# Performance work log

Measured on AMD Instinct MI355X. Metric: run time of the kernel, lower is better.

Reference implementation:

```python
import jax, jax.numpy as jnp
import numpy as np

N_NODES, N_EDGES = 50000, 800000
IN_DIM, OUT_DIM, EDGE_DIM = 128, 128, 32
NUM_HEADS = 8
HEAD_DIM = OUT_DIM // NUM_HEADS
SCALE = HEAD_DIM ** -0.5


def setup_inputs() -> dict:
    key = jax.random.key(0)
    ks = jax.random.split(key, 8)
    def lin_w(k, fan_in, fan_out):
        # kaiming-uniform-ish init like nn.Linear
        bound = 1.0 / np.sqrt(fan_in)
        return jax.random.uniform(k, (fan_in, fan_out), jnp.float32, -bound, bound)
    return {
        "node_features": jax.random.normal(ks[0], (N_NODES, IN_DIM), jnp.float32),
        "edge_features": jax.random.normal(ks[1], (N_EDGES, EDGE_DIM), jnp.float32),
        "Wq": lin_w(ks[2], IN_DIM, OUT_DIM), "bq": jnp.zeros((OUT_DIM,), jnp.float32),
        "Wk": lin_w(ks[3], IN_DIM, OUT_DIM), "bk": jnp.zeros((OUT_DIM,), jnp.float32),
        "Wv": lin_w(ks[4], IN_DIM, OUT_DIM), "bv": jnp.zeros((OUT_DIM,), jnp.float32),
        "We": lin_w(ks[5], EDGE_DIM, OUT_DIM), "be": jnp.zeros((OUT_DIM,), jnp.float32),
        "edge_list": jax.random.randint(ks[6], (N_EDGES, 2), 0, N_NODES, jnp.int32),
        "num_nodes": N_NODES,
    }


def reference(node_features, edge_features, Wq, bq, Wk, bk, Wv, bv, We, be, edge_list, num_nodes):
    # node projections -> [N, H, D]
    Q = (node_features @ Wq + bq).reshape(-1, NUM_HEADS, HEAD_DIM)
    K = (node_features @ Wk + bk).reshape(-1, NUM_HEADS, HEAD_DIM)
    V = (node_features @ Wv + bv).reshape(-1, NUM_HEADS, HEAD_DIM)
    edge_bias = (edge_features @ We + be).reshape(-1, NUM_HEADS, HEAD_DIM)

    src = edge_list[:, 0]  # node_in
    dst = edge_list[:, 1]  # node_out

    # per-edge per-head scores: [E, H]
    scores = jnp.einsum("ehd,ehd->eh", Q[src], K[dst]) * SCALE + edge_bias.sum(-1)
    # NOTE: softmax over the HEADS axis (dim=1), exactly as in the source
    weights = jax.nn.softmax(scores, axis=1)

    # weighted messages gathered from src, scattered to dst: [E, H, D] -> [N, H, D]
    msg = V[src] * weights[..., None]
    node_updates = jax.ops.segment_sum(msg, dst, num_segments=num_nodes)
    return node_updates.reshape(num_nodes, OUT_DIM)
```

## Files before the change

### kernel.cpp

```cpp
#include <hip/hip_runtime.h>
#include <math.h>

#define IN_DIM   128
#define OUT_DIM  128
#define EDGE_DIM 32
#define NUM_HEADS 8
#define HEAD_DIM 16
#define SCALE 0.25f

typedef __attribute__((ext_vector_type(8))) short bf16x8;
typedef __attribute__((ext_vector_type(4))) float f32x4;
typedef __attribute__((ext_vector_type(4))) unsigned int u32x4;

__device__ inline unsigned short f2bf(float x) {
    unsigned int u = __float_as_uint(x);
    unsigned int r = u + 0x7fff + ((u >> 16) & 1);
    return (unsigned short)(r >> 16);
}
__device__ inline float bflo(unsigned int u) { return __uint_as_float(u << 16); }
__device__ inline float bfhi(unsigned int u) { return __uint_as_float(u & 0xffff0000u); }

__global__ __launch_bounds__(256) void setup_kernel(
    int* __restrict__ counts, int n_nodes, int nbz,
    const float* __restrict__ Wq, const float* __restrict__ Wk,
    const float* __restrict__ Wv, unsigned short* __restrict__ WtB, int nbw,
    const float* __restrict__ We, const float* __restrict__ be,
    float* __restrict__ WeR, float* __restrict__ beR,
    const float* __restrict__ X, unsigned short* __restrict__ Xb)
{
    const int bx = blockIdx.x;
    const int t  = threadIdx.x;
    if (bx < nbz) {
        const int i = bx * 256 + t;
        if (i < n_nodes) counts[i] = 0;
    } else if (bx < nbz + nbw) {
        const int idx = (bx - nbz) * 256 + t;
        const int mat = idx >> 14;
        const int rem = idx & 16383;
        const int n = rem >> 7, k = rem & 127;
        const float* W = (mat == 0) ? Wq : (mat == 1) ? Wk : Wv;
        WtB[mat * 16384 + n * 128 + k] = f2bf(W[k * 128 + n]);
    } else if (bx == nbz + nbw) {
        const int k = t >> 3, h = t & 7;
        float s = 0.f;
#pragma unroll
        for (int d = 0; d < HEAD_DIM; ++d) s += We[k * OUT_DIM + h * HEAD_DIM + d];
        WeR[k * NUM_HEADS + h] = s;
        if (t < NUM_HEADS) {
            float sb = 0.f;
#pragma unroll
            for (int d = 0; d < HEAD_DIM; ++d) sb += be[t * HEAD_DIM + d];
            beR[t] = sb;
        }
    } else {
        const int i = (bx - (nbz + nbw + 1)) * 256 + t;
        if (i < n_nodes * 16) {
            const f32x4* xr = (const f32x4*)(X + (size_t)i * 8);
            const f32x4 x0 = xr[0], x1 = xr[1];
            u32x4 p;
            p[0] = (unsigned)f2bf(x0[0]) | ((unsigned)f2bf(x0[1]) << 16);
            p[1] = (unsigned)f2bf(x0[2]) | ((unsigned)f2bf(x0[3]) << 16);
            p[2] = (unsigned)f2bf(x1[0]) | ((unsigned)f2bf(x1[1]) << 16);
            p[3] = (unsigned)f2bf(x1[2]) | ((unsigned)f2bf(x1[3]) << 16);
            *(u32x4*)(Xb + (size_t)i * 8) = p;
        }
    }
}

__global__ __launch_bounds__(256) void mega_kernel(
    const unsigned short* __restrict__ Xb, const unsigned short* __restrict__ WtB,
    const float* __restrict__ bq, const float* __restrict__ bk,
    const float* __restrict__ bv,
    unsigned short* __restrict__ QVb, unsigned short* __restrict__ Kb,
    int n_nodes, int nbq,
    const int* __restrict__ el, int* __restrict__ counts,
    int* __restrict__ rank, int n_edges)
{
    const int bx = blockIdx.x;
    const int t  = threadIdx.x;

    if (bx >= nbq) {
        const int e = (bx - nbq) * 256 + t;
        if (e < n_edges) {
            const int2 ed = ((const int2*)el)[e];
            rank[e] = atomicAdd(&counts[ed.y], 1);
        }
        return;
    }

    __shared__ unsigned short stg[4][16][136];

    const int wave = t >> 6, lane = t & 63;
    const int quad = lane >> 4, li = lane & 15;
    const int m0 = bx * 64 + wave * 16;
    int mrow = m0 + li;
    if (mrow >= n_nodes) mrow = n_nodes - 1;

    bf16x8 a[4];
#pragma unroll
    for (int ks = 0; ks < 4; ++ks)
        a[ks] = *(const bf16x8*)(Xb + (size_t)mrow * 128 + ks * 32 + quad * 8);

    const int R = lane >> 2;
    const int cc = lane & 3;
    const int node = m0 + R;

#pragma unroll
    for (int which = 0; which < 3; ++which) {
        const float* bias = (which == 0) ? bq : (which == 1) ? bk : bv;
        const unsigned short* Wg = WtB + which * 16384;

        f32x4 acc[8];
#pragma unroll
        for (int nt = 0; nt < 8; ++nt) acc[nt] = (f32x4){0.f, 0.f, 0.f, 0.f};

#pragma unroll
        for (int ks = 0; ks < 4; ++ks) {
#pragma unroll
            for (int nt = 0; nt < 8; ++nt) {
                const bf16x8 b = *(const bf16x8*)(Wg + (nt * 16 + li) * 128 + ks * 32 + quad * 8);
                acc[nt] = __builtin_amdgcn_mfma_f32_16x16x32_bf16(a[ks], b, acc[nt], 0, 0, 0);
            }
        }

#pragma unroll
        for (int nt = 0; nt < 8; ++nt) {
            const float bb = bias[nt * 16 + li];
#pragma unroll
            for (int r = 0; r < 4; ++r)
                stg[wave][quad * 4 + r][nt * 16 + li] = f2bf(acc[nt][r] + bb);
        }
        __syncthreads();

        if (node < n_nodes) {
            const u32x4* s = (const u32x4*)(&stg[wave][R][cc * 32]);
            u32x4 d0 = s[0], d1 = s[1], d2 = s[2], d3 = s[3];
            unsigned short* dp =
                (which == 0) ? (QVb + (size_t)node * 256 + cc * 32)
              : (which == 1) ? (Kb  + (size_t)node * 128 + cc * 32)
              :                (QVb + (size_t)node * 256 + 128 + cc * 32);
            u32x4* d = (u32x4*)dp;
            d[0] = d0; d[1] = d1; d[2] = d2; d[3] = d3;
        }
        __syncthreads();
    }
}

__global__ __launch_bounds__(256) void scan1_kernel(
    const int* __restrict__ counts, int* __restrict__ bsums, int n)
{
    __shared__ int lds[256];
    const int i = blockIdx.x * 256 + threadIdx.x;
    lds[threadIdx.x] = (i < n) ? counts[i] : 0;
    __syncthreads();
    for (int off = 128; off > 0; off >>= 1) {
        if (threadIdx.x < off) lds[threadIdx.x] += lds[threadIdx.x + off];
        __syncthreads();
    }
    if (threadIdx.x == 0) bsums[blockIdx.x] = lds[0];
}

__global__ __launch_bounds__(256) void scan3_kernel(
    const int* __restrict__ counts, const int* __restrict__ bsums,
    int* __restrict__ offsets, int n, int n_edges, int nb)
{
    __shared__ int lds[256];
    const int t = threadIdx.x;

    int v = (t < nb) ? bsums[t] : 0;
    lds[t] = v;
    __syncthreads();
    for (int off = 1; off < 256; off <<= 1) {
        const int u = (t >= off) ? lds[t - off] : 0;
        __syncthreads();
        lds[t] += u;
        __syncthreads();
    }
    const int base = (blockIdx.x > 0) ? lds[blockIdx.x - 1] : 0;
    __syncthreads();

    const int i = blockIdx.x * 256 + t;
    const int c = (i < n) ? counts[i] : 0;
    lds[t] = c;
    __syncthreads();
    for (int off = 1; off < 256; off <<= 1) {
        const int u = (t >= off) ? lds[t - off] : 0;
        __syncthreads();
        lds[t] += u;
        __syncthreads();
    }
    if (i < n) offsets[i] = base + lds[t] - c;
    if (blockIdx.x == 0 && t == 0) offsets[n] = n_edges;
}

__global__ __launch_bounds__(256) void scatter_kernel(
    const int* __restrict__ el, const int* __restrict__ rank,
    const float* __restrict__ ef,
    const float* __restrict__ WeR, const float* __restrict__ beR,
    const int* __restrict__ offsets, unsigned int* __restrict__ recs,
    int n_edges)
{
    const int e = blockIdx.x * 256 + threadIdx.x;
    if (e >= n_edges) return;
    const int2 ed = ((const int2*)el)[e];
    const int pos = offsets[ed.y] + rank[e];

    float acc[NUM_HEADS];
#pragma unroll
    for (int h = 0; h < NUM_HEADS; ++h) acc[h] = beR[h];

    const f32x4* efr = (const f32x4*)(ef + (size_t)e * EDGE_DIM);
#pragma unroll
    for (int kk = 0; kk < 8; ++kk) {
        const f32x4 f = efr[kk];
#pragma unroll
        for (int c = 0; c < 4; ++c) {
            const float* wr = WeR + (kk * 4 + c) * NUM_HEADS;
#pragma unroll
            for (int h = 0; h < NUM_HEADS; ++h)
                acc[h] = fmaf(f[c], wr[h], acc[h]);
        }
    }

    u32x4 r0, r1;
    r0[0] = (unsigned)ed.x;
    r0[1] = 0;
    r0[2] = (unsigned)f2bf(acc[0]) | ((unsigned)f2bf(acc[1]) << 16);
    r0[3] = (unsigned)f2bf(acc[2]) | ((unsigned)f2bf(acc[3]) << 16);
    r1[0] = (unsigned)f2bf(acc[4]) | ((unsigned)f2bf(acc[5]) << 16);
    r1[1] = (unsigned)f2bf(acc[6]) | ((unsigned)f2bf(acc[7]) << 16);
    r1[2] = 0; r1[3] = 0;
    u32x4* rp = (u32x4*)(recs + (size_t)pos * 8);
    rp[0] = r0;
    rp[1] = r1;
}

__global__ __launch_bounds__(256) void aggregate_kernel(
    const unsigned short* __restrict__ QVb, const unsigned short* __restrict__ Kb,
    const int* __restrict__ offsets, const unsigned int* __restrict__ recs,
    float* __restrict__ out, int n_nodes)
{
    const int gw   = (blockIdx.x * 256 + threadIdx.x) >> 6;
    const int lane = threadIdx.x & 63;
    const int half = lane >> 5, ln = lane & 31;
    const int node = gw * 2 + half;
    const int h = ln >> 2;
    const bool valid = node < n_nodes;

    int beg = 0, end = 0;
    if (valid) { beg = offsets[node]; end = offsets[node + 1]; }
    const int cnt = end - beg;
    const int mcnt = max(cnt, __shfl_xor(cnt, 32));

    float k0 = 0.f, k1 = 0.f, k2 = 0.f, k3 = 0.f;
    if (valid) {
        const uint2 kp = ((const uint2*)(Kb + (size_t)node * 128))[ln];
        k0 = bflo(kp.x); k1 = bfhi(kp.x); k2 = bflo(kp.y); k3 = bfhi(kp.y);
    }

    float a0 = 0.f, a1 = 0.f, a2 = 0.f, a3 = 0.f;

    uint2 qp = make_uint2(0, 0), vp = make_uint2(0, 0);
    float eb = 0.f;
    if (cnt > 0) {
        const unsigned int* rb = recs + (size_t)beg * 8;
        const int src = (int)rb[0];
        const unsigned int ebp = rb[2 + (h >> 1)];
        eb = (h & 1) ? bfhi(ebp) : bflo(ebp);
        const uint2* r = (const uint2*)(QVb + (size_t)src * 256);
        qp = r[ln];
        vp = r[32 + ln];
    }

    for (int i = 0; i < mcnt; ++i) {
        uint2 nqp = qp, nvp = vp;
        float neb = eb;
        if (i + 1 < cnt) {
            const unsigned int* rb = recs + (size_t)(beg + i + 1) * 8;
            const int ns = (int)rb[0];
            const unsigned int ebp = rb[2 + (h >> 1)];
            neb = (h & 1) ? bfhi(ebp) : bflo(ebp);
            const uint2* r = (const uint2*)(QVb + (size_t)ns * 256);
            nqp = r[ln];
            nvp = r[32 + ln];
        }

        const float q0 = bflo(qp.x), q1 = bfhi(qp.x);
        const float q2 = bflo(qp.y), q3 = bfhi(qp.y);
        float p = fmaf(q0, k0, fmaf(q1, k1, fmaf(q2, k2, q3 * k3)));
        p += __shfl_xor(p, 1);
        p += __shfl_xor(p, 2);
        const float score = fmaf(p, SCALE, eb);

        float mx = score;
        mx = fmaxf(mx, __shfl_xor(mx, 4));
        mx = fmaxf(mx, __shfl_xor(mx, 8));
        mx = fmaxf(mx, __shfl_xor(mx, 16));
        const float ex = __expf(score - mx);
        float den = ex;
        den += __shfl_xor(den, 4);
        den += __shfl_xor(den, 8);
        den += __shfl_xor(den, 16);
        const float w = __fdividef(ex, den);

        if (i < cnt) {
            a0 = fmaf(w, bflo(vp.x), a0);
            a1 = fmaf(w, bfhi(vp.x), a1);
            a2 = fmaf(w, bflo(vp.y), a2);
            a3 = fmaf(w, bfhi(vp.y), a3);
        }
        qp = nqp; vp = nvp; eb = neb;
    }

    if (valid) {
        f32x4 o; o[0] = a0; o[1] = a1; o[2] = a2; o[3] = a3;
        *(((f32x4*)(out + (size_t)node * OUT_DIM)) + ln) = o;
    }
}

extern "C" void kernel_launch(void* const* d_in, const int* in_sizes, int n_in,
                              void* d_out, int out_size, void* d_ws, size_t ws_size,
                              hipStream_t stream)
{
    const float* X   = (const float*)d_in[0];
    const float* ef  = (const float*)d_in[1];
    const float* Wq  = (const float*)d_in[2];
    const float* bq  = (const float*)d_in[3];
    const float* Wk  = (const float*)d_in[4];
    const float* bk  = (const float*)d_in[5];
    const float* Wv  = (const float*)d_in[6];
    const float* bv  = (const float*)d_in[7];
    const float* We  = (const float*)d_in[8];
    const float* be  = (const float*)d_in[9];
    const int*   el  = (const int*)d_in[10];

    const int n_nodes = in_sizes[0] / IN_DIM;
    const int n_edges = in_sizes[10] / 2;

    char* w = (char*)d_ws;
    auto alloc = [&](size_t bytes) { char* p = w; w += (bytes + 255) & ~(size_t)255; return p; };

    unsigned short* QVb    = (unsigned short*)alloc((size_t)n_nodes * 256 * 2);
    unsigned short* Kb     = (unsigned short*)alloc((size_t)n_nodes * 128 * 2);
    unsigned short* WtB    = (unsigned short*)alloc((size_t)3 * 128 * 128 * 2);
    unsigned short* Xb     = (unsigned short*)alloc((size_t)n_nodes * 128 * 2);
    unsigned int*   recs   = (unsigned int*)alloc((size_t)n_edges * 32);
    int* rank    = (int*)alloc((size_t)n_edges * 4);
    float* WeR   = (float*)alloc(EDGE_DIM * NUM_HEADS * 4);
    float* beR   = (float*)alloc(NUM_HEADS * 4);
    int* counts  = (int*)alloc((size_t)n_nodes * 4);
    int* offsets = (int*)alloc((size_t)(n_nodes + 1) * 4);
    int* bsums   = (int*)alloc(256 * 4);

    const int nbz = (n_nodes + 255) / 256;
    const int nbw = (3 * 128 * 128) / 256;
    const int nbx = (n_nodes * 16 + 255) / 256;
    setup_kernel<<<nbz + nbw + 1 + nbx, 256, 0, stream>>>(
        counts, n_nodes, nbz, Wq, Wk, Wv, WtB, nbw, We, be, WeR, beR, X, Xb);

    const int nbh = (n_edges + 255) / 256;
    const int nbq = (n_nodes + 63) / 64;
    mega_kernel<<<nbq + nbh, 256, 0, stream>>>(
        Xb, WtB, bq, bk, bv, QVb, Kb, n_nodes, nbq,
        el, counts, rank, n_edges);

    const int nb = (n_nodes + 255) / 256;
    scan1_kernel<<<nb, 256, 0, stream>>>(counts, bsums, n_nodes);
    scan3_kernel<<<nb, 256, 0, stream>>>(counts, bsums, offsets, n_nodes, n_edges, nb);

    scatter_kernel<<<nbh, 256, 0, stream>>>(
        el, rank, ef, WeR, beR, offsets, recs, n_edges);

    const int nwaves = (n_nodes + 1) / 2;
    aggregate_kernel<<<(nwaves * 64 + 255) / 256, 256, 0, stream>>>(
        QVb, Kb, offsets, recs, (float*)d_out, n_nodes);
}
```

Baseline: 384.3 us.

## Split QKV GEMM per weight with LDS-staged weights; move edge-bias projection into histogram pass

The projection kernel now gives each block one weight matrix (Q, K or V). It stages that 128x128 bf16 weight in LDS with an XOR swizzle and computes 256 rows per block as 4x8 MFMA tiles, reusing each B fragment across four A tiles. Before, each block reread all three weights from global for only 64 rows. The per-edge edge-bias projection moves out of the scatter kernel into the edge/atomic-count blocks of the same launch and is written as 16 bytes per edge. This takes the ef read and FMA work off the scatter critical path, at the cost of an extra 12.8MB write and read. The bf16 X buffer now aliases the recs buffer to save workspace, which is safe only because scatter runs after the GEMM.

```diff
diff --git a/kernel.cpp b/kernel.cpp
--- a/kernel.cpp
+++ b/kernel.cpp
@@ -72,73 +72,122 @@
     const float* __restrict__ bq, const float* __restrict__ bk,
     const float* __restrict__ bv,
     unsigned short* __restrict__ QVb, unsigned short* __restrict__ Kb,
-    int n_nodes, int nbq,
-    const int* __restrict__ el, int* __restrict__ counts,
-    int* __restrict__ rank, int n_edges)
-{
+    int n_nodes, int nbm,
+    const int* __restrict__ el, int* __restrict__ counts, int* __restrict__ rank,
+    const float* __restrict__ ef, const float* __restrict__ WeR,
+    const float* __restrict__ beR, unsigned int* __restrict__ ebias_e,
+    int n_edges)
+{
+    __shared__ unsigned short shW[16384];
     const int bx = blockIdx.x;
     const int t  = threadIdx.x;
-
-    if (bx >= nbq) {
-        const int e = (bx - nbq) * 256 + t;
-        if (e < n_edges) {
-            const int2 ed = ((const int2*)el)[e];
-            rank[e] = atomicAdd(&counts[ed.y], 1);
-        }
+    const int ngemm = 3 * nbm;
+
+    if (bx >= ngemm) {
+        const int e = (bx - ngemm) * 256 + t;
+        if (e >= n_edges) return;
+        const int2 ed = ((const int2*)el)[e];
+        rank[e] = atomicAdd(&counts[ed.y], 1);
+
+        float acc[NUM_HEADS];
+#pragma unroll
+        for (int h = 0; h < NUM_HEADS; ++h) acc[h] = beR[h];
+
+        const f32x4* efr = (const f32x4*)(ef + (size_t)e * EDGE_DIM);
+#pragma unroll
+        for (int kk = 0; kk < 8; ++kk) {
+            const f32x4 f = efr[kk];
+#pragma unroll
+            for (int c = 0; c < 4; ++c) {
+                const float* wr = WeR + (kk * 4 + c) * NUM_HEADS;
+#pragma unroll
+                for (int h = 0; h < NUM_HEADS; ++h)
+                    acc[h] = fmaf(f[c], wr[h], acc[h]);
+            }
+        }
+        u32x4 pk;
+        pk[0] = (unsigned)f2bf(acc[0]) | ((unsigned)f2bf(acc[1]) << 16);
+        pk[1] = (unsigned)f2bf(acc[2]) | ((unsigned)f2bf(acc[3]) << 16);
+        pk[2] = (unsigned)f2bf(acc[4]) | ((unsigned)f2bf(acc[5]) << 16);
+        pk[3] = (unsigned)f2bf(acc[6]) | ((unsigned)f2bf(acc[7]) << 16);
+        *(u32x4*)(ebias_e + (size_t)e * 4) = pk;
         return;
     }
 
-    __shared__ unsigned short stg[4][16][136];
+    const int which = bx / nbm;
+    const int mb    = bx - which * nbm;
+    const unsigned short* Wg = WtB + which * 16384;
+
+#pragma unroll
+    for (int kk = 0; kk < 8; ++kk) {
+        const int c = kk * 256 + t;
+        const u32x4 v = ((const u32x4*)Wg)[c];
+        const int row = c >> 4;
+        const int bir = (c & 15) << 4;
+        *(u32x4*)((char*)shW + row * 256 + (bir ^ ((row & 7) << 4))) = v;
+    }
+    __syncthreads();
 
     const int wave = t >> 6, lane = t & 63;
     const int quad = lane >> 4, li = lane & 15;
-    const int m0 = bx * 64 + wave * 16;
-    int mrow = m0 + li;
-    if (mrow >= n_nodes) mrow = n_nodes - 1;
-
-    bf16x8 a[4];
-#pragma unroll
-    for (int ks = 0; ks < 4; ++ks)
-        a[ks] = *(const bf16x8*)(Xb + (size_t)mrow * 128 + ks * 32 + quad * 8);
-
-    const int R = lane >> 2;
-    const int cc = lane & 3;
-    const int node = m0 + R;
-
-#pragma unroll
-    for (int which = 0; which < 3; ++which) {
-        const float* bias = (which == 0) ? bq : (which == 1) ? bk : bv;
-        const unsigned short* Wg = WtB + which * 16384;
-
-        f32x4 acc[8];
-#pragma unroll
-        for (int nt = 0; nt < 8; ++nt) acc[nt] = (f32x4){0.f, 0.f, 0.f, 0.f};
-
-#pragma unroll
-        for (int ks = 0; ks < 4; ++ks) {
-#pragma unroll
-            for (int nt = 0; nt < 8; ++nt) {
-                const bf16x8 b = *(const bf16x8*)(Wg + (nt * 16 + li) * 128 + ks * 32 + quad * 8);
-                acc[nt] = __builtin_amdgcn_mfma_f32_16x16x32_bf16(a[ks], b, acc[nt], 0, 0, 0);
-            }
-        }
-
+    const int mbase = mb * 256 + wave * 64;
+
+    int mrow[4];
+#pragma unroll
+    for (int m = 0; m < 4; ++m) {
+        const int r_ = mbase + m * 16 + li;
+        mrow[m] = (r_ < n_nodes) ? r_ : (n_nodes - 1);
+    }
+
+    f32x4 acc[4][8];
+#pragma unroll
+    for (int m = 0; m < 4; ++m)
+#pragma unroll
+        for (int nt = 0; nt < 8; ++nt) acc[m][nt] = (f32x4){0.f, 0.f, 0.f, 0.f};
+
+#pragma unroll
+    for (int ks = 0; ks < 4; ++ks) {
+        bf16x8 a[4];
+#pragma unroll
+        for (int m = 0; m < 4; ++m)
+            a[m] = *(const bf16x8*)(Xb + (size_t)mrow[m] * 128 + ks * 32 + quad * 8);
 #pragma unroll
         for (int nt = 0; nt < 8; ++nt) {
-            const float bb = bias[nt * 16 + li];
+            const int row = nt * 16 + li;
+            const bf16x8 b = *(const bf16x8*)((const char*)shW + row * 256 +
+                                ((ks * 64 + quad * 16) ^ ((row & 7) << 4)));
+#pragma unroll
+            for (int m = 0; m < 4; ++m)
+                acc[m][nt] = __builtin_amdgcn_mfma_f32_16x16x32_bf16(a[m], b, acc[m][nt], 0, 0, 0);
+        }
+    }
+
+    const float* bias = (which == 0) ? bq : (which == 1) ? bk : bv;
+    float bv8[8];
+#pragma unroll
+    for (int nt = 0; nt < 8; ++nt) bv8[nt] = bias[nt * 16 + li];
+
+    __syncthreads();
+
+    unsigned short* stg = shW + wave * 2176;
+    const int R = lane >> 2, cc4 = lane & 3;
+#pragma unroll
+    for (int m = 0; m < 4; ++m) {
+#pragma unroll
+        for (int nt = 0; nt < 8; ++nt)
 #pragma unroll
             for (int r = 0; r < 4; ++r)
-                stg[wave][quad * 4 + r][nt * 16 + li] = f2bf(acc[nt][r] + bb);
-        }
-        __syncthreads();
-
+                stg[(quad * 4 + r) * 136 + nt * 16 + li] = f2bf(acc[m][nt][r] + bv8[nt]);
+        __syncthreads();
+
+        const int node = mbase + m * 16 + R;
         if (node < n_nodes) {
-            const u32x4* s = (const u32x4*)(&stg[wave][R][cc * 32]);
+            const u32x4* s = (const u32x4*)(stg + R * 136 + cc4 * 32);
             u32x4 d0 = s[0], d1 = s[1], d2 = s[2], d3 = s[3];
             unsigned short* dp =
-                (which == 0) ? (QVb + (size_t)node * 256 + cc * 32)
-              : (which == 1) ? (Kb  + (size_t)node * 128 + cc * 32)
-              :                (QVb + (size_t)node * 256 + 128 + cc * 32);
+                (which == 0) ? (QVb + (size_t)node * 256 + cc4 * 32)
+              : (which == 1) ? (Kb  + (size_t)node * 128 + cc4 * 32)
+              :                (QVb + (size_t)node * 256 + 128 + cc4 * 32);
             u32x4* d = (u32x4*)dp;
             d[0] = d0; d[1] = d1; d[2] = d2; d[3] = d3;
         }
@@ -195,40 +244,23 @@
 
 __global__ __launch_bounds__(256) void scatter_kernel(
     const int* __restrict__ el, const int* __restrict__ rank,
-    const float* __restrict__ ef,
-    const float* __restrict__ WeR, const float* __restrict__ beR,
+    const unsigned int* __restrict__ ebias_e,
     const int* __restrict__ offsets, unsigned int* __restrict__ recs,
     int n_edges)
 {
     const int e = blockIdx.x * 256 + threadIdx.x;
     if (e >= n_edges) return;
     const int2 ed = ((const int2*)el)[e];
+    const u32x4 eb = *(const u32x4*)(ebias_e + (size_t)e * 4);
     const int pos = offsets[ed.y] + rank[e];
-
-    float acc[NUM_HEADS];
-#pragma unroll
-    for (int h = 0; h < NUM_HEADS; ++h) acc[h] = beR[h];
-
-    const f32x4* efr = (const f32x4*)(ef + (size_t)e * EDGE_DIM);
-#pragma unroll
-    for (int kk = 0; kk < 8; ++kk) {
-        const f32x4 f = efr[kk];
-#pragma unroll
-        for (int c = 0; c < 4; ++c) {
-            const float* wr = WeR + (kk * 4 + c) * NUM_HEADS;
-#pragma unroll
-            for (int h = 0; h < NUM_HEADS; ++h)
-                acc[h] = fmaf(f[c], wr[h], acc[h]);
-        }
-    }
 
     u32x4 r0, r1;
     r0[0] = (unsigned)ed.x;
     r0[1] = 0;
-    r0[2] = (unsigned)f2bf(acc[0]) | ((unsigned)f2bf(acc[1]) << 16);
-    r0[3] = (unsigned)f2bf(acc[2]) | ((unsigned)f2bf(acc[3]) << 16);
-    r1[0] = (unsigned)f2bf(acc[4]) | ((unsigned)f2bf(acc[5]) << 16);
-    r1[1] = (unsigned)f2bf(acc[6]) | ((unsigned)f2bf(acc[7]) << 16);
+    r0[2] = eb[0];
+    r0[3] = eb[1];
+    r1[0] = eb[2];
+    r1[1] = eb[3];
     r1[2] = 0; r1[3] = 0;
     u32x4* rp = (u32x4*)(recs + (size_t)pos * 8);
     rp[0] = r0;
@@ -343,8 +375,8 @@
     unsigned short* QVb    = (unsigned short*)alloc((size_t)n_nodes * 256 * 2);
     unsigned short* Kb     = (unsigned short*)alloc((size_t)n_nodes * 128 * 2);
     unsigned short* WtB    = (unsigned short*)alloc((size_t)3 * 128 * 128 * 2);
-    unsigned short* Xb     = (unsigned short*)alloc((size_t)n_nodes * 128 * 2);
     unsigned int*   recs   = (unsigned int*)alloc((size_t)n_edges * 32);
+    unsigned int*   ebias_e= (unsigned int*)alloc((size_t)n_edges * 16);
     int* rank    = (int*)alloc((size_t)n_edges * 4);
     float* WeR   = (float*)alloc(EDGE_DIM * NUM_HEADS * 4);
     float* beR   = (float*)alloc(NUM_HEADS * 4);
@@ -352,24 +384,26 @@
     int* offsets = (int*)alloc((size_t)(n_nodes + 1) * 4);
     int* bsums   = (int*)alloc(256 * 4);
 
+    unsigned short* Xb = (unsigned short*)recs;
+
     const int nbz = (n_nodes + 255) / 256;
     const int nbw = (3 * 128 * 128) / 256;
     const int nbx = (n_nodes * 16 + 255) / 256;
     setup_kernel<<<nbz + nbw + 1 + nbx, 256, 0, stream>>>(
         counts, n_nodes, nbz, Wq, Wk, Wv, WtB, nbw, We, be, WeR, beR, X, Xb);
 
+    const int nbm = (n_nodes + 255) / 256;
     const int nbh = (n_edges + 255) / 256;
-    const int nbq = (n_nodes + 63) / 64;
-    mega_kernel<<<nbq + nbh, 256, 0, stream>>>(
-        Xb, WtB, bq, bk, bv, QVb, Kb, n_nodes, nbq,
-        el, counts, rank, n_edges);
+    mega_kernel<<<3 * nbm + nbh, 256, 0, stream>>>(
+        Xb, WtB, bq, bk, bv, QVb, Kb, n_nodes, nbm,
+        el, counts, rank, ef, WeR, beR, ebias_e, n_edges);
 
     const int nb = (n_nodes + 255) / 256;
     scan1_kernel<<<nb, 256, 0, stream>>>(counts, bsums, n_nodes);
     scan3_kernel<<<nb, 256, 0, stream>>>(counts, bsums, offsets, n_nodes, n_edges, nb);
 
     scatter_kernel<<<nbh, 256, 0, stream>>>(
-        el, rank, ef, WeR, beR, offsets, recs, n_edges);
+        el, rank, ebias_e, offsets, recs, n_edges);
 
     const int nwaves = (n_nodes + 1) / 2;
     aggregate_kernel<<<(nwaves * 64 + 255) / 256, 256, 0, stream>>>(
```

New measurement: 335.4 us. -12.7%, faster.
